# Performance work log

Measured on AMD Instinct MI355X. Metric: run time of the kernel, lower is better.

Reference implementation:

```python
import jax, jax.numpy as jnp
import numpy as np

B, T, D, V = 32, 384, 768, 32000
PAD = 1
THRESH = 0.95

def setup_inputs() -> dict:
    key = jax.random.key(0)
    ks = jax.random.split(key, 8)
    s = 1.0 / np.sqrt(D)
    sentence = jax.random.randint(ks[0], (B, T), 0, V)
    emb = jax.random.normal(ks[1], (V, D), jnp.float32) * 0.02
    emb = emb.at[PAD].set(0.0)  # padding_idx row is zero
    w_ih = jax.random.uniform(ks[2], (3 * D, D), jnp.float32, -s, s)
    w_hh = jax.random.uniform(ks[3], (3 * D, D), jnp.float32, -s, s)
    b_ih = jax.random.uniform(ks[4], (3 * D,), jnp.float32, -s, s)
    b_hh = jax.random.uniform(ks[5], (3 * D,), jnp.float32, -s, s)
    w_act = jax.random.uniform(ks[6], (D,), jnp.float32, -s, s)
    b_act = jnp.zeros((1,), jnp.float32)
    return dict(sentence=sentence, emb=emb, w_ih=w_ih, w_hh=w_hh,
                b_ih=b_ih, b_hh=b_hh, w_act=w_act, b_act=b_act)


def _gru(x, w_ih, w_hh, b_ih, b_hh):
    # x: [B,T,D] -> states [B,T,D]; PyTorch GRU cell math.
    xp = jnp.einsum('btd,ed->bte', x, w_ih) + b_ih  # [B,T,3D]

    def step(h, xt):
        hp = h @ w_hh.T + b_hh
        xr, xz, xn = jnp.split(xt, 3, axis=-1)
        hr, hz, hn = jnp.split(hp, 3, axis=-1)
        r = jax.nn.sigmoid(xr + hr)
        z = jax.nn.sigmoid(xz + hz)
        n = jnp.tanh(xn + r * hn)
        h_new = (1.0 - z) * n + z * h
        return h_new, h_new

    h0 = jnp.zeros((x.shape[0], w_hh.shape[1]), x.dtype)
    _, hs = jax.lax.scan(step, h0, jnp.swapaxes(xp, 0, 1))
    return jnp.swapaxes(hs, 0, 1)


def _forward(sentence, emb, w_ih, w_hh, b_ih, b_hh, w_act, b_act):
    x = emb[sentence]                                   # [B,T,D]
    states = _gru(x, w_ih, w_hh, b_ih, b_hh)            # [B,T,D]
    probs = jax.nn.sigmoid(states @ w_act + b_act)      # [B,T]

    # ACT-style halting: accumulate probs, emit a segment when sum > threshold.
    def halt_step(hsum, p):
        acc = hsum + p
        halted = acc > THRESH
        return jnp.where(halted, 0.0, acc), halted

    _, halted_t = jax.lax.scan(halt_step, jnp.zeros((B,), probs.dtype), probs.T)
    halted = halted_t.T                                 # [B,T] bool, True at last step of each segment
    h_i = halted.astype(jnp.int32)
    seg_id = jnp.cumsum(h_i, axis=1) - h_i              # exclusive cumsum: segment index per step

    segsum = jax.vmap(lambda v, s: jax.ops.segment_sum(v, s, num_segments=T))
    sum_p = segsum(probs, seg_id)                       # [B,T] per-segment prob sum
    sum_p_at = jnp.take_along_axis(sum_p, seg_id, axis=1)
    # last step of a segment gets weight p_last - stopgrad(sum_seg - 1)
    weights = jnp.where(halted, probs - jax.lax.stop_gradient(sum_p_at - 1.0), probs)
    seg_embs = segsum(states * weights[..., None], seg_id)  # [B,T,D]

    n_segs = h_i.sum(axis=1)                            # [B] completed segments
    valid = jnp.arange(T)[None, :] < n_segs[:, None]    # [B,T]
    embs = jnp.where(valid[..., None], seg_embs, 0.0)   # zero-pad incomplete slots
    embs = embs.reshape(B * T, D)                       # concat padded per-batch lists
    return embs, probs[..., None]


def reference(sentence, emb, w_ih, w_hh, b_ih, b_hh, w_act, b_act):
    return _forward(sentence, emb, w_ih, w_hh, b_ih, b_hh, w_act, b_act)
```

## Files before the change

### kernel.cpp

```cpp
#include <hip/hip_runtime.h>
#include <math.h>

#define BATCH 32
#define SEQT 384
#define DIM 768
#define D3 2304
#define NROWS (BATCH*SEQT)
#define VTHRESH 0.95f

typedef float  f32x4 __attribute__((ext_vector_type(4)));

#define OFF_XP   ((size_t)0)
#define SZ_XP    ((size_t)NROWS * D3 * 4)
#define OFF_ST   (OFF_XP + SZ_XP)
#define SZ_ST    ((size_t)NROWS * DIM * 4)
#define OFF_PR   (OFF_ST + SZ_ST)
#define SZ_PR    ((size_t)NROWS * 4)
#define OFF_WT   (OFF_PR + SZ_PR)
#define OFF_SS   (OFF_WT + SZ_PR)
#define OFF_SE   (OFF_SS + SZ_PR)
#define OFF_NS   (OFF_SE + SZ_PR)
#define OFF_HB   (OFF_NS + 256)
#define NBG 8
#define BPG 4
#define WPB 32
#define CPW 24
#define BGBYTES ((size_t)(DIM * 2 * 16))
#define SZ_HB   ((size_t)2 * NBG * BGBYTES)
#define INIT_FLOATS (SZ_HB/4)

#define DOT4(a,b) ((a).x*(b).x + (a).y*(b).y + (a).z*(b).z + (a).w*(b).w)

__global__ __launch_bounds__(256, 2) void k_xp(
    const int* __restrict__ sent, const float* __restrict__ emb,
    const float* __restrict__ w_ih, const float* __restrict__ b_ih,
    float* __restrict__ xp)
{
    __shared__ float As[16][132];
    __shared__ float Bs[16][132];
    const int tid = threadIdx.x;
    const int mt = blockIdx.x, nt = blockIdx.y;
    const int tx = tid & 15, ty = tid >> 4;
    const int lm = tid >> 2;
    const int lk = (tid & 3) << 2;

    const long arow0 = (long)sent[mt*128 + lm] * DIM;
    const long arow1 = (long)sent[mt*128 + lm + 64] * DIM;
    const float* b0p = w_ih + (size_t)(nt*128 + lm) * DIM;
    const float* b1p = w_ih + (size_t)(nt*128 + lm + 64) * DIM;

    float acc[8][8];
    #pragma unroll
    for (int i = 0; i < 8; ++i)
        #pragma unroll
        for (int j = 0; j < 8; ++j) acc[i][j] = 0.f;

    for (int k0 = 0; k0 < DIM; k0 += 16) {
        float4 a0 = *(const float4*)(emb + arow0 + k0 + lk);
        float4 a1 = *(const float4*)(emb + arow1 + k0 + lk);
        float4 b0 = *(const float4*)(b0p + k0 + lk);
        float4 b1 = *(const float4*)(b1p + k0 + lk);
        __syncthreads();
        As[lk+0][lm] = a0.x; As[lk+1][lm] = a0.y; As[lk+2][lm] = a0.z; As[lk+3][lm] = a0.w;
        As[lk+0][lm+64] = a1.x; As[lk+1][lm+64] = a1.y; As[lk+2][lm+64] = a1.z; As[lk+3][lm+64] = a1.w;
        Bs[lk+0][lm] = b0.x; Bs[lk+1][lm] = b0.y; Bs[lk+2][lm] = b0.z; Bs[lk+3][lm] = b0.w;
        Bs[lk+0][lm+64] = b1.x; Bs[lk+1][lm+64] = b1.y; Bs[lk+2][lm+64] = b1.z; Bs[lk+3][lm+64] = b1.w;
        __syncthreads();
        #pragma unroll
        for (int k = 0; k < 16; ++k) {
            float4 av0 = *(const float4*)&As[k][ty*8];
            float4 av1 = *(const float4*)&As[k][ty*8+4];
            float4 bv0 = *(const float4*)&Bs[k][tx*8];
            float4 bv1 = *(const float4*)&Bs[k][tx*8+4];
            float a[8] = {av0.x,av0.y,av0.z,av0.w,av1.x,av1.y,av1.z,av1.w};
            float b[8] = {bv0.x,bv0.y,bv0.z,bv0.w,bv1.x,bv1.y,bv1.z,bv1.w};
            #pragma unroll
            for (int i = 0; i < 8; ++i)
                #pragma unroll
                for (int j = 0; j < 8; ++j)
                    acc[i][j] += a[i]*b[j];
        }
    }

    const int m0 = mt*128 + ty*8;
    const int n0 = nt*128 + tx*8;
    float4 bi0 = *(const float4*)(b_ih + n0);
    float4 bi1 = *(const float4*)(b_ih + n0 + 4);
    #pragma unroll
    for (int i = 0; i < 8; ++i) {
        float4 v0, v1;
        v0.x = acc[i][0] + bi0.x; v0.y = acc[i][1] + bi0.y;
        v0.z = acc[i][2] + bi0.z; v0.w = acc[i][3] + bi0.w;
        v1.x = acc[i][4] + bi1.x; v1.y = acc[i][5] + bi1.y;
        v1.z = acc[i][6] + bi1.z; v1.w = acc[i][7] + bi1.w;
        *(float4*)(xp + (size_t)(m0+i)*D3 + n0)     = v0;
        *(float4*)(xp + (size_t)(m0+i)*D3 + n0 + 4) = v1;
    }
}

#define HPITCH 772

__global__ __launch_bounds__(384, 1) void k_gru(
    const float* __restrict__ w_hh, const float* __restrict__ b_hh,
    const float* __restrict__ xp, float* __restrict__ states,
    char* __restrict__ hbuf)
{
    __shared__ float h_lds[2][BPG][HPITCH];

    const int tid = threadIdx.x;
    const int jb  = blockIdx.x & 31;
    const int bg  = blockIdx.x >> 5;
    const int w    = tid >> 6;
    const int lane = tid & 63;
    const int g    = lane >> 4;
    const int c16  = lane & 15;
    const int col  = jb*CPW + w*4 + g;
    const int bloc = c16 >> 2;
    const int batch = bg*BPG + bloc;

    float4 w4[3][12];
    #pragma unroll
    for (int g3 = 0; g3 < 3; ++g3) {
        const float* wr = w_hh + (size_t)(g3*DIM + col)*DIM + c16*4;
        #pragma unroll
        for (int m = 0; m < 12; ++m)
            w4[g3][m] = *(const float4*)(wr + m*64);
    }
    const float bhr = b_hh[col];
    const float bhz = b_hh[DIM + col];
    const float bhn = b_hh[2*DIM + col];

    int goff[4], ldsoff[4], onemask = 0;
    #pragma unroll
    for (int i = 0; i < 4; ++i) {
        int q = i*384 + tid;
        int cq = q >> 1, sq = q & 1;
        goff[i]   = q << 4;
        ldsoff[i] = (sq ? 3 : 0)*HPITCH + cq;
        if (sq) onemask |= (1<<i);
    }

    char* pb[2];
    pb[0] = hbuf + (size_t)(0*NBG + bg)*BGBYTES;
    pb[1] = hbuf + (size_t)(1*NBG + bg)*BGBYTES;

    const float* xq = xp + (size_t)batch*SEQT*D3 + col;

    f32x4 ch[4];

#define ISSUE_POLLS(pbx)                                                 \
    {                                                                    \
        _Pragma("unroll")                                                \
        for (int k = 0; k < 4; ++k) {                                    \
            const f32x4* ap = (const f32x4*)((pbx) + goff[k]);           \
            asm volatile("global_load_dwordx4 %0, %1, off sc0 sc1"       \
                         : "=v"(ch[k]) : "v"(ap));                       \
        }                                                                \
    }

#define WAIT_FILL(pbx, hb0, tt)                                          \
    {                                                                    \
        asm volatile("s_waitcnt vmcnt(0)" ::: "memory");                 \
        __builtin_amdgcn_sched_barrier(0);                               \
        int need = 15;                                                   \
        _Pragma("unroll")                                                \
        for (int k = 0; k < 4; ++k)                                      \
            if (__float_as_int(ch[k].w) == (tt)) need &= ~(1<<k);        \
        while (need) {                                                   \
            _Pragma("unroll")                                            \
            for (int k = 0; k < 4; ++k)                                  \
                if (need & (1<<k)) {                                     \
                    const f32x4* ap = (const f32x4*)((pbx) + goff[k]);   \
                    asm volatile("global_load_dwordx4 %0, %1, off sc0 sc1"\
                                 : "=v"(ch[k]) : "v"(ap));               \
                }                                                        \
            asm volatile("s_waitcnt vmcnt(0)" ::: "memory");             \
            __builtin_amdgcn_sched_barrier(0);                           \
            _Pragma("unroll")                                            \
            for (int k = 0; k < 4; ++k)                                  \
                if ((need & (1<<k)) && __float_as_int(ch[k].w) == (tt))  \
                    need &= ~(1<<k);                                     \
            if (need) __builtin_amdgcn_s_sleep(1);                       \
        }                                                                \
        _Pragma("unroll")                                                \
        for (int k = 0; k < 4; ++k) {                                    \
            (hb0)[ldsoff[k]] = ch[k].x;                                  \
            if (!((onemask >> k) & 1)) {                                 \
                (hb0)[ldsoff[k] + HPITCH]   = ch[k].y;                   \
                (hb0)[ldsoff[k] + 2*HPITCH] = ch[k].z;                   \
            }                                                            \
        }                                                                \
    }

#define GRU_GATES(xr, xz, xn, ar, az, an)                                \
    {                                                                    \
        float rg = 1.f / (1.f + expf(-((xr) + (ar) + bhr)));             \
        float zg = 1.f / (1.f + expf(-((xz) + (az) + bhz)));             \
        float ng = tanhf((xn) + rg * ((an) + bhn));                      \
        hold = (1.f - zg) * ng + zg * hold;                              \
    }

#define PUBLISH(pbx, tt)                                                 \
    {                                                                    \
        int gp = (lane >> 1) & 3;                                        \
        int sq = lane & 1;                                               \
        float q0 = __shfl(hold, gp*16 + (sq ? 12 : 0));                  \
        float q1 = __shfl(hold, gp*16 + 4);                              \
        float q2 = __shfl(hold, gp*16 + 8);                              \
        if (lane < 8) {                                                  \
            f32x4 val;                                                   \
            val.x = q0; val.y = q1; val.z = q2;                          \
            val.w = __int_as_float((tt) + 1);                            \
            int colp = jb*CPW + w*4 + gp;                                \
            f32x4* ap = (f32x4*)((pbx) + (size_t)(colp*2 + sq)*16);      \
            asm volatile("global_store_dwordx4 %0, %1, off sc0 sc1"      \
                         :: "v"(ap), "v"(val) : "memory");               \
        }                                                                \
        if ((c16 & 3) == 0)                                              \
            states[(size_t)(batch*SEQT + (tt))*DIM + col] = hold;        \
    }

    float hold = 0.f;

    float xr = xq[0], xz = xq[DIM], xn = xq[2*DIM];
    GRU_GATES(xr, xz, xn, 0.f, 0.f, 0.f);
    PUBLISH(pb[0], 0);
    ISSUE_POLLS(pb[0]);
    float xrn = xq[(size_t)D3], xzn = xq[(size_t)D3 + DIM],
          xnn = xq[(size_t)D3 + 2*DIM];

    for (int t = 1; t < SEQT; ++t) {
        float* hb0 = &h_lds[t & 1][0][0];
        WAIT_FILL(pb[(t-1)&1], hb0, t);
        xr = xrn; xz = xzn; xn = xnn;
        if (t + 1 < SEQT) {
            xrn = xq[(size_t)(t+1)*D3];
            xzn = xq[(size_t)(t+1)*D3 + DIM];
            xnn = xq[(size_t)(t+1)*D3 + 2*DIM];
        }
        __syncthreads();

        float v[12];
        #pragma unroll
        for (int i = 0; i < 12; ++i) v[i] = 0.f;
        const float* hk = hb0 + c16*4;
        #pragma unroll
        for (int bb = 0; bb < 4; ++bb) {
            const float* hr = hk + bb*HPITCH;
            #pragma unroll
            for (int m = 0; m < 12; ++m) {
                float4 h4 = *(const float4*)(hr + m*64);
                v[bb*3+0] += DOT4(h4, w4[0][m]);
                v[bb*3+1] += DOT4(h4, w4[1][m]);
                v[bb*3+2] += DOT4(h4, w4[2][m]);
            }
        }
        #pragma unroll
        for (int i = 0; i < 6; ++i) {
            float send = (c16 & 8) ? v[i] : v[i+6];
            float keep = (c16 & 8) ? v[i+6] : v[i];
            v[i] = keep + __shfl_xor(send, 8);
        }
        #pragma unroll
        for (int i = 0; i < 3; ++i) {
            float send = (c16 & 4) ? v[i] : v[i+3];
            float keep = (c16 & 4) ? v[i+3] : v[i];
            v[i] = keep + __shfl_xor(send, 4);
        }
        #pragma unroll
        for (int i = 0; i < 3; ++i) v[i] += __shfl_xor(v[i], 2);
        #pragma unroll
        for (int i = 0; i < 3; ++i) v[i] += __shfl_xor(v[i], 1);

        GRU_GATES(xr, xz, xn, v[0], v[1], v[2]);
        PUBLISH(pb[t&1], t);
        if (t + 1 < SEQT)
            ISSUE_POLLS(pb[t&1]);
    }
#undef ISSUE_POLLS
#undef WAIT_FILL
#undef GRU_GATES
#undef PUBLISH
}

__global__ __launch_bounds__(256, 4) void k_probs(
    const float* __restrict__ states, const float* __restrict__ w_act,
    const float* __restrict__ b_act, float* __restrict__ probs,
    float* __restrict__ out_probs)
{
    int row  = blockIdx.x*4 + (threadIdx.x >> 6);
    int lane = threadIdx.x & 63;
    const float* sr = states + (size_t)row * DIM;
    float s = 0.f;
    #pragma unroll
    for (int i = 0; i < 3; ++i) {
        float4 v = *(const float4*)(sr + i*256 + lane*4);
        float4 w = *(const float4*)(w_act + i*256 + lane*4);
        s += v.x*w.x + v.y*w.y + v.z*w.z + v.w*w.w;
    }
    #pragma unroll
    for (int off = 32; off > 0; off >>= 1) s += __shfl_xor(s, off);
    if (lane == 0) {
        float pv = 1.f / (1.f + expf(-(s + b_act[0])));
        probs[row]     = pv;
        out_probs[row] = pv;
    }
}

__global__ void k_scan(const float* __restrict__ probs, float* __restrict__ weights,
                       int* __restrict__ seg_start, int* __restrict__ seg_end,
                       int* __restrict__ n_segs)
{
    int b = threadIdx.x;
    if (b >= BATCH) return;
    float acc = 0.f;
    int s = 0, start = 0;
    for (int t0 = 0; t0 < SEQT; t0 += 4) {
        float4 p4 = *(const float4*)(probs + b*SEQT + t0);
        float pv[4] = {p4.x, p4.y, p4.z, p4.w};
        #pragma unroll
        for (int k = 0; k < 4; ++k) {
            int t = t0 + k;
            float pp = pv[k];
            acc += pp;
            float w = pp;
            if (acc > VTHRESH) {
                w = pp - (acc - 1.0f);
                seg_start[b*SEQT + s] = start;
                seg_end[b*SEQT + s]   = t;
                s++; start = t + 1; acc = 0.f;
            }
            weights[b*SEQT + t] = w;
        }
    }
    n_segs[b] = s;
}

__global__ __launch_bounds__(256, 4) void k_embs(
    const float* __restrict__ states, const float* __restrict__ weights,
    const int* __restrict__ seg_start, const int* __restrict__ seg_end,
    const int* __restrict__ n_segs, float* __restrict__ out)
{
    int r = blockIdx.x;
    int b = r / SEQT;
    int s = r - b*SEQT;
    int tid = threadIdx.x;
    float a0 = 0.f, a1 = 0.f, a2 = 0.f;
    if (s < n_segs[b]) {
        int st = seg_start[r], en = seg_end[r];
        for (int t = st; t <= en; ++t) {
            float w = weights[b*SEQT + t];
            const float* sp = states + (size_t)(b*SEQT + t) * DIM;
            a0 += w * sp[tid];
            a1 += w * sp[tid + 256];
            a2 += w * sp[tid + 512];
        }
    }
    float* o = out + (size_t)r * DIM;
    o[tid]       = a0;
    o[tid + 256] = a1;
    o[tid + 512] = a2;
}

__global__ void k_init(float* hb) {
    int i = blockIdx.x * 256 + threadIdx.x;
    if (i < INIT_FLOATS) hb[i] = 0.f;
}

extern "C" void kernel_launch(void* const* d_in, const int* in_sizes, int n_in,
                              void* d_out, int out_size, void* d_ws, size_t ws_size,
                              hipStream_t stream)
{
    const int*   sent  = (const int*)d_in[0];
    const float* emb   = (const float*)d_in[1];
    const float* w_ih  = (const float*)d_in[2];
    const float* w_hh  = (const float*)d_in[3];
    const float* b_ih  = (const float*)d_in[4];
    const float* b_hh  = (const float*)d_in[5];
    const float* w_act = (const float*)d_in[6];
    const float* b_act = (const float*)d_in[7];
    float* out = (float*)d_out;

    char* ws = (char*)d_ws;
    float* xp      = (float*)(ws + OFF_XP);
    float* states  = (float*)(ws + OFF_ST);
    float* probs   = (float*)(ws + OFF_PR);
    float* weights = (float*)(ws + OFF_WT);
    int*   sstart  = (int*)(ws + OFF_SS);
    int*   send    = (int*)(ws + OFF_SE);
    int*   nsegs   = (int*)(ws + OFF_NS);
    char*  hbuf    = (char*)(ws + OFF_HB);

    k_init<<<384, 256, 0, stream>>>((float*)hbuf);
    k_xp<<<dim3(96, 18), 256, 0, stream>>>(sent, emb, w_ih, b_ih, xp);
    k_gru<<<256, 384, 0, stream>>>(w_hh, b_hh, xp, states, hbuf);
    k_probs<<<NROWS/4, 256, 0, stream>>>(states, w_act, b_act, probs,
                                         out + (size_t)NROWS * DIM);
    k_scan<<<1, 64, 0, stream>>>(probs, weights, sstart, send, nsegs);
    k_embs<<<NROWS, 256, 0, stream>>>(states, weights, sstart, send, nsegs, out);
}
```

Before: 2.383 ms.

## Split each GRU column dot product across 32 lanes with 768-thread blocks

Doubles the threads per block of the persistent GRU recurrence kernel from 384 to 768. Each column's hidden-to-hidden dot product is now split across 32 lanes instead of 16, which halves the weight registers and the LDS reads per thread and adds one more shuffle-reduction stage. The aim is to shorten the per-timestep critical path and give the hardware more waves to hide latency. The costs are more synchronisation participants per block, an extra reduction step, and more contention in the polling and publish traffic.

```diff
diff --git a/kernel.cpp b/kernel.cpp
--- a/kernel.cpp
+++ b/kernel.cpp
@@ -100,7 +100,7 @@
 
 #define HPITCH 772
 
-__global__ __launch_bounds__(384, 1) void k_gru(
+__global__ __launch_bounds__(768, 1) void k_gru(
     const float* __restrict__ w_hh, const float* __restrict__ b_hh,
     const float* __restrict__ xp, float* __restrict__ states,
     char* __restrict__ hbuf)
@@ -112,28 +112,28 @@
     const int bg  = blockIdx.x >> 5;
     const int w    = tid >> 6;
     const int lane = tid & 63;
-    const int g    = lane >> 4;
-    const int c16  = lane & 15;
-    const int col  = jb*CPW + w*4 + g;
-    const int bloc = c16 >> 2;
+    const int half = lane >> 5;
+    const int c32  = lane & 31;
+    const int col  = jb*CPW + w*2 + half;
+    const int bloc = (c32 >> 3) & 3;
     const int batch = bg*BPG + bloc;
 
-    float4 w4[3][12];
+    f32x4 w4[3][6];
     #pragma unroll
     for (int g3 = 0; g3 < 3; ++g3) {
-        const float* wr = w_hh + (size_t)(g3*DIM + col)*DIM + c16*4;
-        #pragma unroll
-        for (int m = 0; m < 12; ++m)
-            w4[g3][m] = *(const float4*)(wr + m*64);
+        const float* wr = w_hh + (size_t)(g3*DIM + col)*DIM + c32*4;
+        #pragma unroll
+        for (int m = 0; m < 6; ++m)
+            w4[g3][m] = *(const f32x4*)(wr + m*128);
     }
     const float bhr = b_hh[col];
     const float bhz = b_hh[DIM + col];
     const float bhn = b_hh[2*DIM + col];
 
-    int goff[4], ldsoff[4], onemask = 0;
-    #pragma unroll
-    for (int i = 0; i < 4; ++i) {
-        int q = i*384 + tid;
+    int goff[2], ldsoff[2], onemask = 0;
+    #pragma unroll
+    for (int i = 0; i < 2; ++i) {
+        int q = i*768 + tid;
         int cq = q >> 1, sq = q & 1;
         goff[i]   = q << 4;
         ldsoff[i] = (sq ? 3 : 0)*HPITCH + cq;
@@ -146,12 +146,12 @@
 
     const float* xq = xp + (size_t)batch*SEQT*D3 + col;
 
-    f32x4 ch[4];
+    f32x4 ch[2];
 
 #define ISSUE_POLLS(pbx)                                                 \
     {                                                                    \
         _Pragma("unroll")                                                \
-        for (int k = 0; k < 4; ++k) {                                    \
+        for (int k = 0; k < 2; ++k) {                                    \
             const f32x4* ap = (const f32x4*)((pbx) + goff[k]);           \
             asm volatile("global_load_dwordx4 %0, %1, off sc0 sc1"       \
                          : "=v"(ch[k]) : "v"(ap));                       \
@@ -162,13 +162,13 @@
     {                                                                    \
         asm volatile("s_waitcnt vmcnt(0)" ::: "memory");                 \
         __builtin_amdgcn_sched_barrier(0);                               \
-        int need = 15;                                                   \
+        int need = 3;                                                    \
         _Pragma("unroll")                                                \
-        for (int k = 0; k < 4; ++k)                                      \
+        for (int k = 0; k < 2; ++k)                                      \
             if (__float_as_int(ch[k].w) == (tt)) need &= ~(1<<k);        \
         while (need) {                                                   \
             _Pragma("unroll")                                            \
-            for (int k = 0; k < 4; ++k)                                  \
+            for (int k = 0; k < 2; ++k)                                  \
                 if (need & (1<<k)) {                                     \
                     const f32x4* ap = (const f32x4*)((pbx) + goff[k]);   \
                     asm volatile("global_load_dwordx4 %0, %1, off sc0 sc1"\
@@ -177,13 +177,13 @@
             asm volatile("s_waitcnt vmcnt(0)" ::: "memory");             \
             __builtin_amdgcn_sched_barrier(0);                           \
             _Pragma("unroll")                                            \
-            for (int k = 0; k < 4; ++k)                                  \
+            for (int k = 0; k < 2; ++k)                                  \
                 if ((need & (1<<k)) && __float_as_int(ch[k].w) == (tt))  \
                     need &= ~(1<<k);                                     \
             if (need) __builtin_amdgcn_s_sleep(1);                       \
         }                                                                \
         _Pragma("unroll")                                                \
-        for (int k = 0; k < 4; ++k) {                                    \
+        for (int k = 0; k < 2; ++k) {                                    \
             (hb0)[ldsoff[k]] = ch[k].x;                                  \
             if (!((onemask >> k) & 1)) {                                 \
                 (hb0)[ldsoff[k] + HPITCH]   = ch[k].y;                   \
@@ -202,21 +202,21 @@
 
 #define PUBLISH(pbx, tt)                                                 \
     {                                                                    \
-        int gp = (lane >> 1) & 3;                                        \
+        int gp = (lane >> 1) & 1;                                        \
         int sq = lane & 1;                                               \
-        float q0 = __shfl(hold, gp*16 + (sq ? 12 : 0));                  \
-        float q1 = __shfl(hold, gp*16 + 4);                              \
-        float q2 = __shfl(hold, gp*16 + 8);                              \
-        if (lane < 8) {                                                  \
+        float q0 = __shfl(hold, gp*32 + (sq ? 24 : 0));                  \
+        float q1 = __shfl(hold, gp*32 + 8);                              \
+        float q2 = __shfl(hold, gp*32 + 16);                             \
+        if (lane < 4) {                                                  \
             f32x4 val;                                                   \
             val.x = q0; val.y = q1; val.z = q2;                          \
             val.w = __int_as_float((tt) + 1);                            \
-            int colp = jb*CPW + w*4 + gp;                                \
+            int colp = jb*CPW + w*2 + gp;                                \
             f32x4* ap = (f32x4*)((pbx) + (size_t)(colp*2 + sq)*16);      \
             asm volatile("global_store_dwordx4 %0, %1, off sc0 sc1"      \
                          :: "v"(ap), "v"(val) : "memory");               \
         }                                                                \
-        if ((c16 & 3) == 0)                                              \
+        if ((c32 & 7) == 0)                                              \
             states[(size_t)(batch*SEQT + (tt))*DIM + col] = hold;        \
     }
 
@@ -243,13 +243,13 @@
         float v[12];
         #pragma unroll
         for (int i = 0; i < 12; ++i) v[i] = 0.f;
-        const float* hk = hb0 + c16*4;
+        const float* hk = hb0 + c32*4;
         #pragma unroll
         for (int bb = 0; bb < 4; ++bb) {
             const float* hr = hk + bb*HPITCH;
             #pragma unroll
-            for (int m = 0; m < 12; ++m) {
-                float4 h4 = *(const float4*)(hr + m*64);
+            for (int m = 0; m < 6; ++m) {
+                f32x4 h4 = *(const f32x4*)(hr + m*128);
                 v[bb*3+0] += DOT4(h4, w4[0][m]);
                 v[bb*3+1] += DOT4(h4, w4[1][m]);
                 v[bb*3+2] += DOT4(h4, w4[2][m]);
@@ -257,16 +257,18 @@
         }
         #pragma unroll
         for (int i = 0; i < 6; ++i) {
-            float send = (c16 & 8) ? v[i] : v[i+6];
-            float keep = (c16 & 8) ? v[i+6] : v[i];
+            float send = (c32 & 16) ? v[i] : v[i+6];
+            float keep = (c32 & 16) ? v[i+6] : v[i];
+            v[i] = keep + __shfl_xor(send, 16);
+        }
+        #pragma unroll
+        for (int i = 0; i < 3; ++i) {
+            float send = (c32 & 8) ? v[i] : v[i+3];
+            float keep = (c32 & 8) ? v[i+3] : v[i];
             v[i] = keep + __shfl_xor(send, 8);
         }
         #pragma unroll
-        for (int i = 0; i < 3; ++i) {
-            float send = (c16 & 4) ? v[i] : v[i+3];
-            float keep = (c16 & 4) ? v[i+3] : v[i];
-            v[i] = keep + __shfl_xor(send, 4);
-        }
+        for (int i = 0; i < 3; ++i) v[i] += __shfl_xor(v[i], 4);
         #pragma unroll
         for (int i = 0; i < 3; ++i) v[i] += __shfl_xor(v[i], 2);
         #pragma unroll
@@ -393,7 +395,7 @@
 
     k_init<<<384, 256, 0, stream>>>((float*)hbuf);
     k_xp<<<dim3(96, 18), 256, 0, stream>>>(sent, emb, w_ih, b_ih, xp);
-    k_gru<<<256, 384, 0, stream>>>(w_hh, b_hh, xp, states, hbuf);
+    k_gru<<<256, 768, 0, stream>>>(w_hh, b_hh, xp, states, hbuf);
     k_probs<<<NROWS/4, 256, 0, stream>>>(states, w_act, b_act, probs,
                                          out + (size_t)NROWS * DIM);
     k_scan<<<1, 64, 0, stream>>>(probs, weights, sstart, send, nsegs);
```

Measured after the change: 2.334 ms. 2.1% less time.
